# Kernel tuning notes

Measured on AMD Instinct MI355X. Metric: run time of the kernel, lower is better.

Reference implementation:

```python
import jax, jax.numpy as jnp
import numpy as np

B, D, L, R, O = 32768, 128, 3, 64, 64
EPS = 1e-5


def setup_inputs() -> dict:
    key = jax.random.key(0)
    ks = jax.random.split(key, 5)
    s_in = 1.0 / np.sqrt(D)
    s_r = 1.0 / np.sqrt(R)
    return {
        "x": jax.random.normal(ks[0], (B, D, L), dtype=jnp.float32),
        "layer0": jax.random.uniform(ks[1], (D, R), minval=-s_in, maxval=s_in, dtype=jnp.float32),
        "core1": jax.random.uniform(ks[2], (R, D, R), minval=-s_in, maxval=s_in, dtype=jnp.float32),
        "core2": jax.random.uniform(ks[3], (R, D, R), minval=-s_in, maxval=s_in, dtype=jnp.float32),
        "last": jax.random.uniform(ks[4], (R, O), minval=-s_r, maxval=s_r, dtype=jnp.float32),
        "ln_w": jnp.ones((D, L), dtype=jnp.float32),
        "ln_b": jnp.zeros((D, L), dtype=jnp.float32),
    }


def reference(x, layer0, core1, core2, last, ln_w, ln_b):
    # LayerNorm over the last two dims [D, L] with affine params
    mu = jnp.mean(x, axis=(1, 2), keepdims=True)
    var = jnp.var(x, axis=(1, 2), keepdims=True)
    xn = (x - mu) * jax.lax.rsqrt(var + EPS) * ln_w + ln_b  # [B, D, L]

    # Tensor-train contraction chain. The original builds a khatri-rao
    # [B, R*D] per step then matmuls with the reshaped [R*D, R] core;
    # einsum 'br,bd,rds->bs' computes the identical contraction fused.
    temp = xn[:, :, 0] @ layer0  # [B, R]
    temp = jnp.einsum("br,bd,rds->bs", temp, xn[:, :, 1], core1)
    temp = jnp.einsum("br,bd,rds->bs", temp, xn[:, :, 2], core2)
    return temp @ last  # [B, O]
```

## Files before the change

### kernel.cpp

```cpp
#include <hip/hip_runtime.h>
#include <hip/hip_fp16.h>

typedef _Float16 f16x8 __attribute__((ext_vector_type(8)));
typedef float f32x16 __attribute__((ext_vector_type(16)));

union H2x4 { f16x8 v; __half2 h2[4]; unsigned u[4]; };
union U1H2 { unsigned u; __half2 h; };

#define TB 128
#define XN0_OFF  0
#define RING_OFF 32768
#define T_OFF    65536
#define XN12_OFF 81920
#define SMEM_BYTES 148480
#define WS_CT1   0
#define WS_CT2   1048576
#define WS_L0T   2097152
#define WS_LASTT 2113536

#define WAITBAR0() asm volatile("s_waitcnt vmcnt(0)\n\ts_barrier" ::: "memory")

__device__ __forceinline__ void gload_lds16(const void* g, void* l) {
  __builtin_amdgcn_global_load_lds(
      (const __attribute__((address_space(1))) unsigned int*)g,
      (__attribute__((address_space(3))) unsigned int*)l, 16, 0, 0);
}

__device__ __forceinline__ void issue_chunk16(const unsigned char* g,
                                              unsigned char* l, int tid) {
  gload_lds16(g + tid * 16, l + tid * 16);
}

__device__ __forceinline__ unsigned pack_h2(float a, float b) {
  return (unsigned)__half_as_ushort(__float2half(a)) |
         ((unsigned)__half_as_ushort(__float2half(b)) << 16);
}

__device__ __forceinline__ void reduce_T(unsigned char* smem, f32x16 a0, f32x16 a1,
                                         int p, int kh, int mh, int h, int scol) {
  float* scr = (float*)(smem + (kh ? RING_OFF : XN0_OFF));
  __syncthreads();
  if (p == 0) {
#pragma unroll
    for (int j = 0; j < 16; ++j) {
      const int r0 = (j & 3) + 8 * (j >> 2) + 4 * h;
      const int row = mh * 64 + r0;
      scr[row * 64 + scol] = a0[j];
      scr[(row + 32) * 64 + scol] = a1[j];
    }
  }
  __syncthreads();
  if (p == 1) {
#pragma unroll
    for (int j = 0; j < 16; ++j) {
      const int r0 = (j & 3) + 8 * (j >> 2) + 4 * h;
      const int row = mh * 64 + r0;
      scr[row * 64 + scol] += a0[j];
      scr[(row + 32) * 64 + scol] += a1[j];
    }
  }
  __syncthreads();
  if (p == 0) {
    const float* s0 = (const float*)(smem + XN0_OFF);
    const float* s1 = (const float*)(smem + RING_OFF);
#pragma unroll
    for (int j = 0; j < 16; ++j) {
      const int r0 = (j & 3) + 8 * (j >> 2) + 4 * h;
      const int row = mh * 64 + kh * 32 + r0;
      const float vsum = s0[row * 64 + scol] + s1[row * 64 + scol];
      *(__half*)(smem + T_OFF + row * 128 + ((2 * scol) ^ ((row & 7) << 4))) =
          __float2half(vsum);
    }
  }
  __syncthreads();
}

__global__ void __launch_bounds__(512) tt_prep(
    const float* __restrict__ layer0, const float* __restrict__ core1,
    const float* __restrict__ core2, const float* __restrict__ last,
    unsigned char* __restrict__ ws) {
  const int tid = blockIdx.x * 512 + threadIdx.x;
  if (tid < 524288) {
    const int which = tid >> 18;
    const int w = tid & 262143;
    const float* core = which ? core2 : core1;
    unsigned char* ct = ws + (which ? WS_CT2 : WS_CT1);
    const int d = w >> 11, rem = w & 2047, s = rem >> 5, j = rem & 31, r = 2 * j;
    const unsigned val = pack_h2(core[r * 8192 + d * 64 + s],
                                 core[(r + 1) * 8192 + d * 64 + s]);
    *(unsigned*)(ct + d * 8192 + s * 128 + 4 * (j ^ ((s & 7) << 2))) = val;
  } else if (tid < 528384) {
    const int w = tid - 524288;
    const int r = w >> 6, j = w & 63, d = 2 * j;
    const unsigned val = pack_h2(layer0[d * 64 + r], layer0[(d + 1) * 64 + r]);
    *(unsigned*)(ws + WS_L0T + r * 256 + 4 * j) = val;
  } else if (tid < 530432) {
    const int w = tid - 528384;
    const int o = w >> 5, j = w & 31, r = 2 * j;
    const unsigned val = pack_h2(last[r * 64 + o], last[(r + 1) * 64 + o]);
    *(unsigned*)(ws + WS_LASTT + o * 128 + 4 * j) = val;
  }
}

__global__ void __launch_bounds__(1024, 4) tt_fused(
    const float* __restrict__ x, const float* __restrict__ lnw,
    const float* __restrict__ lnb, const unsigned char* __restrict__ ws,
    float* __restrict__ out) {
  __shared__ alignas(16) unsigned char smem[SMEM_BYTES];
  const int tid = threadIdx.x;
  const int wid = tid >> 6;
  const int lane = tid & 63;
  const int l31 = lane & 31;
  const int h = lane >> 5;
  const int p  = wid & 1;
  const int kh = (wid >> 1) & 1;
  const int sb = (wid >> 2) & 1;
  const int mh = (wid >> 3) & 1;
  const int bg0 = blockIdx.x * TB;
  const int scol = sb * 32 + l31;
  const int sOff = scol * 128;
  const int swzA = (l31 & 7) << 4;

  {
    float wv[6], bv[6];
#pragma unroll
    for (int k = 0; k < 6; ++k) { wv[k] = lnw[lane + 64 * k]; bv[k] = lnb[lane + 64 * k]; }
#pragma unroll
    for (int rr = 0; rr < 8; ++rr) {
      const int row = wid * 8 + rr;
      const float* xrow = x + (size_t)(bg0 + row) * 384;
      float v[6];
#pragma unroll
      for (int k = 0; k < 6; ++k) v[k] = xrow[lane + 64 * k];
      float s = 0.f, ss = 0.f;
#pragma unroll
      for (int k = 0; k < 6; ++k) { s += v[k]; ss += v[k] * v[k]; }
#pragma unroll
      for (int m = 1; m < 64; m <<= 1) { s += __shfl_xor(s, m); ss += __shfl_xor(ss, m); }
      const float mu = s * (1.f / 384.f);
      const float var = ss * (1.f / 384.f) - mu * mu;
      const float rstd = rsqrtf(var + 1e-5f);
#pragma unroll
      for (int k = 0; k < 6; ++k) {
        const int i = lane + 64 * k;
        const int d = i / 3;
        const int sl = i - 3 * d;
        const float xv = (v[k] - mu) * rstd * wv[k] + bv[k];
        if (sl == 0) {
          *(__half*)(smem + XN0_OFF + row * 256 + ((2 * d) ^ ((row & 7) << 4))) =
              __float2half(xv);
        } else {
          *(__half*)(smem + XN12_OFF + d * 520 + 4 * row + 2 * (sl - 1)) =
              __float2half(xv);
        }
      }
    }
  }
  __syncthreads();

  f32x16 acc0, acc1;

#pragma unroll
  for (int i = 0; i < 16; ++i) { acc0[i] = 0.f; acc1[i] = 0.f; }
  {
    const unsigned char* l0t = ws + WS_L0T;
#pragma unroll
    for (int kbL = 0; kbL < 2; ++kbL) {
      const int cb = (((p << 1) | kh) * 2 + kbL) * 32 + h * 16;
      f16x8 bf = *(const f16x8*)(l0t + scol * 256 + cb);
      f16x8 a0 = *(const f16x8*)(smem + XN0_OFF + (mh * 64 + l31) * 256 + (cb ^ swzA));
      f16x8 a1 = *(const f16x8*)(smem + XN0_OFF + (mh * 64 + 32 + l31) * 256 + (cb ^ swzA));
      acc0 = __builtin_amdgcn_mfma_f32_32x32x16_f16(a0, bf, acc0, 0, 0, 0);
      acc1 = __builtin_amdgcn_mfma_f32_32x32x16_f16(a1, bf, acc1, 0, 0, 0);
    }
  }
  reduce_T(smem, acc0, acc1, p, kh, mh, h, scol);

  for (int st = 0; st < 2; ++st) {
    const unsigned char* ctg = ws + (st ? WS_CT2 : WS_CT1);

    issue_chunk16(ctg, smem + RING_OFF, tid);

    H2x4 tp00, tp01, tp10, tp11;
    {
      const int rb0 = kh * 64 + h * 16;
      const int ra = (mh * 64 + l31) * 128;
      const int rb = (mh * 64 + 32 + l31) * 128;
      tp00.v = *(const f16x8*)(smem + T_OFF + ra + (rb0 ^ swzA));
      tp01.v = *(const f16x8*)(smem + T_OFF + ra + ((rb0 + 32) ^ swzA));
      tp10.v = *(const f16x8*)(smem + T_OFF + rb + (rb0 ^ swzA));
      tp11.v = *(const f16x8*)(smem + T_OFF + rb + ((rb0 + 32) ^ swzA));
    }

#pragma unroll
    for (int i = 0; i < 16; ++i) { acc0[i] = 0.f; acc1[i] = 0.f; }

#pragma unroll 1
    for (int cg = 0; cg < 64; ++cg) {
      WAITBAR0();
      if (cg < 63)
        issue_chunk16(ctg + (cg + 1) * 16384,
                      smem + RING_OFF + ((cg + 1) & 1) * 16384, tid);
      const unsigned char* bp =
          smem + RING_OFF + (cg & 1) * 16384 + p * 8192 + sOff;
      const unsigned char* xp = smem + XN12_OFF + (2 * cg + p) * 520 +
                                4 * (mh * 64 + l31) + 2 * st;
      const unsigned xv0 = *(const unsigned short*)xp;
      const unsigned xv1 = *(const unsigned short*)(xp + 128);
      U1H2 d0, d1;
      d0.u = xv0 | (xv0 << 16);
      d1.u = xv1 | (xv1 << 16);
      const int rb = kh * 64 + h * 16;
      {
        f16x8 bf = *(const f16x8*)(bp + (rb ^ swzA));
        H2x4 af0, af1;
#pragma unroll
        for (int i = 0; i < 4; ++i) {
          af0.h2[i] = __hmul2(tp00.h2[i], d0.h);
          af1.h2[i] = __hmul2(tp10.h2[i], d1.h);
        }
        acc0 = __builtin_amdgcn_mfma_f32_32x32x16_f16(af0.v, bf, acc0, 0, 0, 0);
        acc1 = __builtin_amdgcn_mfma_f32_32x32x16_f16(af1.v, bf, acc1, 0, 0, 0);
      }
      {
        f16x8 bf = *(const f16x8*)(bp + ((rb + 32) ^ swzA));
        H2x4 af0, af1;
#pragma unroll
        for (int i = 0; i < 4; ++i) {
          af0.h2[i] = __hmul2(tp01.h2[i], d0.h);
          af1.h2[i] = __hmul2(tp11.h2[i], d1.h);
        }
        acc0 = __builtin_amdgcn_mfma_f32_32x32x16_f16(af0.v, bf, acc0, 0, 0, 0);
        acc1 = __builtin_amdgcn_mfma_f32_32x32x16_f16(af1.v, bf, acc1, 0, 0, 0);
      }
    }
    reduce_T(smem, acc0, acc1, p, kh, mh, h, scol);
  }

  if (p == 0) {
    f32x16 accd;
#pragma unroll
    for (int i = 0; i < 16; ++i) accd[i] = 0.f;
    const unsigned char* lastT = ws + WS_LASTT;
    const int rbase = mh * 64 + kh * 32;
#pragma unroll
    for (int kb = 0; kb < 4; ++kb) {
      const int cb = kb * 32 + h * 16;
      f16x8 bf = *(const f16x8*)(lastT + scol * 128 + cb);
      f16x8 af = *(const f16x8*)(smem + T_OFF + (rbase + l31) * 128 + (cb ^ swzA));
      accd = __builtin_amdgcn_mfma_f32_32x32x16_f16(af, bf, accd, 0, 0, 0);
    }
#pragma unroll
    for (int j = 0; j < 16; ++j) {
      const int r0 = (j & 3) + 8 * (j >> 2) + 4 * h;
      out[(size_t)(bg0 + rbase + r0) * 64 + scol] = accd[j];
    }
  }
}

extern "C" void kernel_launch(void* const* d_in, const int* in_sizes, int n_in,
                              void* d_out, int out_size, void* d_ws, size_t ws_size,
                              hipStream_t stream) {
  const float* x      = (const float*)d_in[0];
  const float* layer0 = (const float*)d_in[1];
  const float* core1  = (const float*)d_in[2];
  const float* core2  = (const float*)d_in[3];
  const float* last   = (const float*)d_in[4];
  const float* lnw    = (const float*)d_in[5];
  const float* lnb    = (const float*)d_in[6];
  unsigned char* ws   = (unsigned char*)d_ws;
  float* outp         = (float*)d_out;

  tt_prep<<<1036, 512, 0, stream>>>(layer0, core1, core2, last, ws);
  tt_fused<<<256, 1024, 0, stream>>>(x, lnw, lnb, ws, outp);
}
```

Measured before the change: 101.5 us.

## Halve block to 512 threads with 4 M-tiles per wave and fragment-ordered core layout

```diff
diff --git a/kernel.cpp b/kernel.cpp
--- a/kernel.cpp
+++ b/kernel.cpp
@@ -29,6 +29,7 @@
 __device__ __forceinline__ void issue_chunk16(const unsigned char* g,
                                               unsigned char* l, int tid) {
   gload_lds16(g + tid * 16, l + tid * 16);
+  gload_lds16(g + tid * 16 + 8192, l + tid * 16 + 8192);
 }
 
 __device__ __forceinline__ unsigned pack_h2(float a, float b) {
@@ -36,17 +37,19 @@
          ((unsigned)__half_as_ushort(__float2half(b)) << 16);
 }
 
-__device__ __forceinline__ void reduce_T(unsigned char* smem, f32x16 a0, f32x16 a1,
-                                         int p, int kh, int mh, int h, int scol) {
+__device__ __forceinline__ void reduce_T(unsigned char* smem,
+                                         f32x16 a0, f32x16 a1, f32x16 a2, f32x16 a3,
+                                         int p, int kh, int h, int scol) {
   float* scr = (float*)(smem + (kh ? RING_OFF : XN0_OFF));
   __syncthreads();
   if (p == 0) {
 #pragma unroll
     for (int j = 0; j < 16; ++j) {
       const int r0 = (j & 3) + 8 * (j >> 2) + 4 * h;
-      const int row = mh * 64 + r0;
-      scr[row * 64 + scol] = a0[j];
-      scr[(row + 32) * 64 + scol] = a1[j];
+      scr[r0 * 64 + scol]        = a0[j];
+      scr[(32 + r0) * 64 + scol] = a1[j];
+      scr[(64 + r0) * 64 + scol] = a2[j];
+      scr[(96 + r0) * 64 + scol] = a3[j];
     }
   }
   __syncthreads();
@@ -54,9 +57,10 @@
 #pragma unroll
     for (int j = 0; j < 16; ++j) {
       const int r0 = (j & 3) + 8 * (j >> 2) + 4 * h;
-      const int row = mh * 64 + r0;
-      scr[row * 64 + scol] += a0[j];
-      scr[(row + 32) * 64 + scol] += a1[j];
+      scr[r0 * 64 + scol]        += a0[j];
+      scr[(32 + r0) * 64 + scol] += a1[j];
+      scr[(64 + r0) * 64 + scol] += a2[j];
+      scr[(96 + r0) * 64 + scol] += a3[j];
     }
   }
   __syncthreads();
@@ -66,8 +70,12 @@
 #pragma unroll
     for (int j = 0; j < 16; ++j) {
       const int r0 = (j & 3) + 8 * (j >> 2) + 4 * h;
-      const int row = mh * 64 + kh * 32 + r0;
-      const float vsum = s0[row * 64 + scol] + s1[row * 64 + scol];
+      int row = kh * 32 + r0;
+      float vsum = s0[row * 64 + scol] + s1[row * 64 + scol];
+      *(__half*)(smem + T_OFF + row * 128 + ((2 * scol) ^ ((row & 7) << 4))) =
+          __float2half(vsum);
+      row += 64;
+      vsum = s0[row * 64 + scol] + s1[row * 64 + scol];
       *(__half*)(smem + T_OFF + row * 128 + ((2 * scol) ^ ((row & 7) << 4))) =
           __float2half(vsum);
     }
@@ -85,10 +93,20 @@
     const int w = tid & 262143;
     const float* core = which ? core2 : core1;
     unsigned char* ct = ws + (which ? WS_CT2 : WS_CT1);
-    const int d = w >> 11, rem = w & 2047, s = rem >> 5, j = rem & 31, r = 2 * j;
-    const unsigned val = pack_h2(core[r * 8192 + d * 64 + s],
-                                 core[(r + 1) * 8192 + d * 64 + s]);
-    *(unsigned*)(ct + d * 8192 + s * 128 + 4 * (j ^ ((s & 7) << 2))) = val;
+    const int j   = w & 3;
+    const int lp  = (w >> 2) & 63;
+    const int blk = w >> 8;
+    const int kbL = blk & 1;
+    const int kh  = (blk >> 1) & 1;
+    const int sb  = (blk >> 2) & 1;
+    const int d   = blk >> 3;
+    const int hh  = lp & 1;
+    const int l31 = lp >> 1;
+    const int s   = sb * 32 + l31;
+    const int r0  = kh * 32 + kbL * 16 + hh * 8 + 2 * j;
+    const unsigned val = pack_h2(core[r0 * 8192 + d * 64 + s],
+                                 core[(r0 + 1) * 8192 + d * 64 + s]);
+    *(unsigned*)(ct + (size_t)w * 4) = val;
   } else if (tid < 528384) {
     const int w = tid - 524288;
     const int r = w >> 6, j = w & 63, d = 2 * j;
@@ -102,7 +120,18 @@
   }
 }
 
-__global__ void __launch_bounds__(1024, 4) tt_fused(
+#define KRSTEP(TPa, TPb, E, ACC)                                              \
+  do {                                                                        \
+    H2x4 af;                                                                  \
+    _Pragma("unroll") for (int q = 0; q < 4; ++q)                             \
+        af.h2[q] = __hmul2(TPa.h2[q], (E).h);                                 \
+    ACC = __builtin_amdgcn_mfma_f32_32x32x16_f16(af.v, bf0, ACC, 0, 0, 0);    \
+    _Pragma("unroll") for (int q = 0; q < 4; ++q)                             \
+        af.h2[q] = __hmul2(TPb.h2[q], (E).h);                                 \
+    ACC = __builtin_amdgcn_mfma_f32_32x32x16_f16(af.v, bf1, ACC, 0, 0, 0);    \
+  } while (0)
+
+__global__ void __launch_bounds__(512, 2) tt_fused(
     const float* __restrict__ x, const float* __restrict__ lnw,
     const float* __restrict__ lnb, const unsigned char* __restrict__ ws,
     float* __restrict__ out) {
@@ -115,10 +144,9 @@
   const int p  = wid & 1;
   const int kh = (wid >> 1) & 1;
   const int sb = (wid >> 2) & 1;
-  const int mh = (wid >> 3) & 1;
   const int bg0 = blockIdx.x * TB;
   const int scol = sb * 32 + l31;
-  const int sOff = scol * 128;
+  const int lp16 = (l31 * 2 + h) * 16;
   const int swzA = (l31 & 7) << 4;
 
   {
@@ -126,8 +154,8 @@
 #pragma unroll
     for (int k = 0; k < 6; ++k) { wv[k] = lnw[lane + 64 * k]; bv[k] = lnb[lane + 64 * k]; }
 #pragma unroll
-    for (int rr = 0; rr < 8; ++rr) {
-      const int row = wid * 8 + rr;
+    for (int rr = 0; rr < 16; ++rr) {
+      const int row = wid * 16 + rr;
       const float* xrow = x + (size_t)(bg0 + row) * 384;
       float v[6];
 #pragma unroll
@@ -158,42 +186,48 @@
   }
   __syncthreads();
 
-  f32x16 acc0, acc1;
-
-#pragma unroll
-  for (int i = 0; i < 16; ++i) { acc0[i] = 0.f; acc1[i] = 0.f; }
+  f32x16 acc0, acc1, acc2, acc3;
+
+#pragma unroll
+  for (int i = 0; i < 16; ++i) { acc0[i] = 0.f; acc1[i] = 0.f; acc2[i] = 0.f; acc3[i] = 0.f; }
   {
     const unsigned char* l0t = ws + WS_L0T;
 #pragma unroll
     for (int kbL = 0; kbL < 2; ++kbL) {
       const int cb = (((p << 1) | kh) * 2 + kbL) * 32 + h * 16;
       f16x8 bf = *(const f16x8*)(l0t + scol * 256 + cb);
-      f16x8 a0 = *(const f16x8*)(smem + XN0_OFF + (mh * 64 + l31) * 256 + (cb ^ swzA));
-      f16x8 a1 = *(const f16x8*)(smem + XN0_OFF + (mh * 64 + 32 + l31) * 256 + (cb ^ swzA));
-      acc0 = __builtin_amdgcn_mfma_f32_32x32x16_f16(a0, bf, acc0, 0, 0, 0);
-      acc1 = __builtin_amdgcn_mfma_f32_32x32x16_f16(a1, bf, acc1, 0, 0, 0);
-    }
-  }
-  reduce_T(smem, acc0, acc1, p, kh, mh, h, scol);
+      f16x8 aA = *(const f16x8*)(smem + XN0_OFF + l31 * 256 + (cb ^ swzA));
+      f16x8 aB = *(const f16x8*)(smem + XN0_OFF + (32 + l31) * 256 + (cb ^ swzA));
+      f16x8 aC = *(const f16x8*)(smem + XN0_OFF + (64 + l31) * 256 + (cb ^ swzA));
+      f16x8 aD = *(const f16x8*)(smem + XN0_OFF + (96 + l31) * 256 + (cb ^ swzA));
+      acc0 = __builtin_amdgcn_mfma_f32_32x32x16_f16(aA, bf, acc0, 0, 0, 0);
+      acc1 = __builtin_amdgcn_mfma_f32_32x32x16_f16(aB, bf, acc1, 0, 0, 0);
+      acc2 = __builtin_amdgcn_mfma_f32_32x32x16_f16(aC, bf, acc2, 0, 0, 0);
+      acc3 = __builtin_amdgcn_mfma_f32_32x32x16_f16(aD, bf, acc3, 0, 0, 0);
+    }
+  }
+  reduce_T(smem, acc0, acc1, acc2, acc3, p, kh, h, scol);
 
   for (int st = 0; st < 2; ++st) {
     const unsigned char* ctg = ws + (st ? WS_CT2 : WS_CT1);
 
     issue_chunk16(ctg, smem + RING_OFF, tid);
 
-    H2x4 tp00, tp01, tp10, tp11;
+    H2x4 tp00, tp01, tp10, tp11, tp20, tp21, tp30, tp31;
     {
       const int rb0 = kh * 64 + h * 16;
-      const int ra = (mh * 64 + l31) * 128;
-      const int rb = (mh * 64 + 32 + l31) * 128;
-      tp00.v = *(const f16x8*)(smem + T_OFF + ra + (rb0 ^ swzA));
-      tp01.v = *(const f16x8*)(smem + T_OFF + ra + ((rb0 + 32) ^ swzA));
-      tp10.v = *(const f16x8*)(smem + T_OFF + rb + (rb0 ^ swzA));
-      tp11.v = *(const f16x8*)(smem + T_OFF + rb + ((rb0 + 32) ^ swzA));
-    }
-
-#pragma unroll
-    for (int i = 0; i < 16; ++i) { acc0[i] = 0.f; acc1[i] = 0.f; }
+      tp00.v = *(const f16x8*)(smem + T_OFF + l31 * 128 + (rb0 ^ swzA));
+      tp01.v = *(const f16x8*)(smem + T_OFF + l31 * 128 + ((rb0 + 32) ^ swzA));
+      tp10.v = *(const f16x8*)(smem + T_OFF + (32 + l31) * 128 + (rb0 ^ swzA));
+      tp11.v = *(const f16x8*)(smem + T_OFF + (32 + l31) * 128 + ((rb0 + 32) ^ swzA));
+      tp20.v = *(const f16x8*)(smem + T_OFF + (64 + l31) * 128 + (rb0 ^ swzA));
+      tp21.v = *(const f16x8*)(smem + T_OFF + (64 + l31) * 128 + ((rb0 + 32) ^ swzA));
+      tp30.v = *(const f16x8*)(smem + T_OFF + (96 + l31) * 128 + (rb0 ^ swzA));
+      tp31.v = *(const f16x8*)(smem + T_OFF + (96 + l31) * 128 + ((rb0 + 32) ^ swzA));
+    }
+
+#pragma unroll
+    for (int i = 0; i < 16; ++i) { acc0[i] = 0.f; acc1[i] = 0.f; acc2[i] = 0.f; acc3[i] = 0.f; }
 
 #pragma unroll 1
     for (int cg = 0; cg < 64; ++cg) {
@@ -201,59 +235,48 @@
       if (cg < 63)
         issue_chunk16(ctg + (cg + 1) * 16384,
                       smem + RING_OFF + ((cg + 1) & 1) * 16384, tid);
-      const unsigned char* bp =
-          smem + RING_OFF + (cg & 1) * 16384 + p * 8192 + sOff;
+      const unsigned char* bp = smem + RING_OFF + (cg & 1) * 16384 +
+                                p * 8192 + sb * 4096 + kh * 2048 + lp16;
+      f16x8 bf0 = *(const f16x8*)(bp);
+      f16x8 bf1 = *(const f16x8*)(bp + 1024);
       const unsigned char* xp = smem + XN12_OFF + (2 * cg + p) * 520 +
-                                4 * (mh * 64 + l31) + 2 * st;
-      const unsigned xv0 = *(const unsigned short*)xp;
+                                4 * l31 + 2 * st;
+      const unsigned xv0 = *(const unsigned short*)(xp);
       const unsigned xv1 = *(const unsigned short*)(xp + 128);
-      U1H2 d0, d1;
-      d0.u = xv0 | (xv0 << 16);
-      d1.u = xv1 | (xv1 << 16);
-      const int rb = kh * 64 + h * 16;
-      {
-        f16x8 bf = *(const f16x8*)(bp + (rb ^ swzA));
-        H2x4 af0, af1;
-#pragma unroll
-        for (int i = 0; i < 4; ++i) {
-          af0.h2[i] = __hmul2(tp00.h2[i], d0.h);
-          af1.h2[i] = __hmul2(tp10.h2[i], d1.h);
-        }
-        acc0 = __builtin_amdgcn_mfma_f32_32x32x16_f16(af0.v, bf, acc0, 0, 0, 0);
-        acc1 = __builtin_amdgcn_mfma_f32_32x32x16_f16(af1.v, bf, acc1, 0, 0, 0);
-      }
-      {
-        f16x8 bf = *(const f16x8*)(bp + ((rb + 32) ^ swzA));
-        H2x4 af0, af1;
-#pragma unroll
-        for (int i = 0; i < 4; ++i) {
-          af0.h2[i] = __hmul2(tp01.h2[i], d0.h);
-          af1.h2[i] = __hmul2(tp11.h2[i], d1.h);
-        }
-        acc0 = __builtin_amdgcn_mfma_f32_32x32x16_f16(af0.v, bf, acc0, 0, 0, 0);
-        acc1 = __builtin_amdgcn_mfma_f32_32x32x16_f16(af1.v, bf, acc1, 0, 0, 0);
-      }
-    }
-    reduce_T(smem, acc0, acc1, p, kh, mh, h, scol);
+      const unsigned xv2 = *(const unsigned short*)(xp + 256);
+      const unsigned xv3 = *(const unsigned short*)(xp + 384);
+      U1H2 e0, e1, e2, e3;
+      e0.u = xv0 | (xv0 << 16);
+      e1.u = xv1 | (xv1 << 16);
+      e2.u = xv2 | (xv2 << 16);
+      e3.u = xv3 | (xv3 << 16);
+      KRSTEP(tp00, tp01, e0, acc0);
+      KRSTEP(tp10, tp11, e1, acc1);
+      KRSTEP(tp20, tp21, e2, acc2);
+      KRSTEP(tp30, tp31, e3, acc3);
+    }
+    reduce_T(smem, acc0, acc1, acc2, acc3, p, kh, h, scol);
   }
 
   if (p == 0) {
-    f32x16 accd;
-#pragma unroll
-    for (int i = 0; i < 16; ++i) accd[i] = 0.f;
+    f32x16 accd0, accd1;
+#pragma unroll
+    for (int i = 0; i < 16; ++i) { accd0[i] = 0.f; accd1[i] = 0.f; }
     const unsigned char* lastT = ws + WS_LASTT;
-    const int rbase = mh * 64 + kh * 32;
 #pragma unroll
     for (int kb = 0; kb < 4; ++kb) {
       const int cb = kb * 32 + h * 16;
       f16x8 bf = *(const f16x8*)(lastT + scol * 128 + cb);
-      f16x8 af = *(const f16x8*)(smem + T_OFF + (rbase + l31) * 128 + (cb ^ swzA));
-      accd = __builtin_amdgcn_mfma_f32_32x32x16_f16(af, bf, accd, 0, 0, 0);
-    }
-#pragma unroll
-    for (int j = 0; j < 16; ++j) {
-      const int r0 = (j & 3) + 8 * (j >> 2) + 4 * h;
-      out[(size_t)(bg0 + rbase + r0) * 64 + scol] = accd[j];
+      f16x8 af0 = *(const f16x8*)(smem + T_OFF + (kh * 32 + l31) * 128 + (cb ^ swzA));
+      f16x8 af1 = *(const f16x8*)(smem + T_OFF + (64 + kh * 32 + l31) * 128 + (cb ^ swzA));
+      accd0 = __builtin_amdgcn_mfma_f32_32x32x16_f16(af0, bf, accd0, 0, 0, 0);
+      accd1 = __builtin_amdgcn_mfma_f32_32x32x16_f16(af1, bf, accd1, 0, 0, 0);
+    }
+#pragma unroll
+    for (int j = 0; j < 16; ++j) {
+      const int r0 = (j & 3) + 8 * (j >> 2) + 4 * h;
+      out[(size_t)(bg0 + kh * 32 + r0) * 64 + scol] = accd0[j];
+      out[(size_t)(bg0 + 64 + kh * 32 + r0) * 64 + scol] = accd1[j];
     }
   }
 }
@@ -272,5 +295,5 @@
   float* outp         = (float*)d_out;
 
   tt_prep<<<1036, 512, 0, stream>>>(layer0, core1, core2, last, ws);
-  tt_fused<<<256, 1024, 0, stream>>>(x, lnw, lnb, ws, outp);
-}
+  tt_fused<<<256, 512, 0, stream>>>(x, lnw, lnb, ws, outp);
+}
```

Result: slower. 104.4 us (+2.9%).

## Pre-permute TT cores into MFMA fragment order and double chunk size

Applied to the files above, without the earlier changes.

```diff
diff --git a/kernel.cpp b/kernel.cpp
--- a/kernel.cpp
+++ b/kernel.cpp
@@ -8,10 +8,10 @@
 union U1H2 { unsigned u; __half2 h; };
 
 #define TB 128
-#define XN0_OFF  0
-#define RING_OFF 32768
-#define T_OFF    65536
-#define XN12_OFF 81920
+#define SLOT0_OFF 0
+#define SLOT1_OFF 32768
+#define T_OFF     65536
+#define XN12_OFF  81920
 #define SMEM_BYTES 148480
 #define WS_CT1   0
 #define WS_CT2   1048576
@@ -26,9 +26,10 @@
       (__attribute__((address_space(3))) unsigned int*)l, 16, 0, 0);
 }
 
-__device__ __forceinline__ void issue_chunk16(const unsigned char* g,
+__device__ __forceinline__ void issue_chunk32(const unsigned char* g,
                                               unsigned char* l, int tid) {
   gload_lds16(g + tid * 16, l + tid * 16);
+  gload_lds16(g + tid * 16 + 16384, l + tid * 16 + 16384);
 }
 
 __device__ __forceinline__ unsigned pack_h2(float a, float b) {
@@ -38,7 +39,7 @@
 
 __device__ __forceinline__ void reduce_T(unsigned char* smem, f32x16 a0, f32x16 a1,
                                          int p, int kh, int mh, int h, int scol) {
-  float* scr = (float*)(smem + (kh ? RING_OFF : XN0_OFF));
+  float* scr = (float*)(smem + (kh ? SLOT1_OFF : SLOT0_OFF));
   __syncthreads();
   if (p == 0) {
 #pragma unroll
@@ -61,8 +62,8 @@
   }
   __syncthreads();
   if (p == 0) {
-    const float* s0 = (const float*)(smem + XN0_OFF);
-    const float* s1 = (const float*)(smem + RING_OFF);
+    const float* s0 = (const float*)(smem + SLOT0_OFF);
+    const float* s1 = (const float*)(smem + SLOT1_OFF);
 #pragma unroll
     for (int j = 0; j < 16; ++j) {
       const int r0 = (j & 3) + 8 * (j >> 2) + 4 * h;
@@ -85,10 +86,20 @@
     const int w = tid & 262143;
     const float* core = which ? core2 : core1;
     unsigned char* ct = ws + (which ? WS_CT2 : WS_CT1);
-    const int d = w >> 11, rem = w & 2047, s = rem >> 5, j = rem & 31, r = 2 * j;
-    const unsigned val = pack_h2(core[r * 8192 + d * 64 + s],
-                                 core[(r + 1) * 8192 + d * 64 + s]);
-    *(unsigned*)(ct + d * 8192 + s * 128 + 4 * (j ^ ((s & 7) << 2))) = val;
+    const int j   = w & 3;
+    const int lp  = (w >> 2) & 63;
+    const int blk = w >> 8;
+    const int kbL = blk & 1;
+    const int kh  = (blk >> 1) & 1;
+    const int sb  = (blk >> 2) & 1;
+    const int d   = blk >> 3;
+    const int hh  = lp & 1;
+    const int l31 = lp >> 1;
+    const int s   = sb * 32 + l31;
+    const int r0  = kh * 32 + kbL * 16 + hh * 8 + 2 * j;
+    const unsigned val = pack_h2(core[r0 * 8192 + d * 64 + s],
+                                 core[(r0 + 1) * 8192 + d * 64 + s]);
+    *(unsigned*)(ct + (size_t)w * 4) = val;
   } else if (tid < 528384) {
     const int w = tid - 524288;
     const int r = w >> 6, j = w & 63, d = 2 * j;
@@ -118,7 +129,7 @@
   const int mh = (wid >> 3) & 1;
   const int bg0 = blockIdx.x * TB;
   const int scol = sb * 32 + l31;
-  const int sOff = scol * 128;
+  const int lp16 = (l31 * 2 + h) * 16;
   const int swzA = (l31 & 7) << 4;
 
   {
@@ -147,7 +158,7 @@
         const int sl = i - 3 * d;
         const float xv = (v[k] - mu) * rstd * wv[k] + bv[k];
         if (sl == 0) {
-          *(__half*)(smem + XN0_OFF + row * 256 + ((2 * d) ^ ((row & 7) << 4))) =
+          *(__half*)(smem + SLOT0_OFF + row * 256 + ((2 * d) ^ ((row & 7) << 4))) =
               __float2half(xv);
         } else {
           *(__half*)(smem + XN12_OFF + d * 520 + 4 * row + 2 * (sl - 1)) =
@@ -168,8 +179,8 @@
     for (int kbL = 0; kbL < 2; ++kbL) {
       const int cb = (((p << 1) | kh) * 2 + kbL) * 32 + h * 16;
       f16x8 bf = *(const f16x8*)(l0t + scol * 256 + cb);
-      f16x8 a0 = *(const f16x8*)(smem + XN0_OFF + (mh * 64 + l31) * 256 + (cb ^ swzA));
-      f16x8 a1 = *(const f16x8*)(smem + XN0_OFF + (mh * 64 + 32 + l31) * 256 + (cb ^ swzA));
+      f16x8 a0 = *(const f16x8*)(smem + SLOT0_OFF + (mh * 64 + l31) * 256 + (cb ^ swzA));
+      f16x8 a1 = *(const f16x8*)(smem + SLOT0_OFF + (mh * 64 + 32 + l31) * 256 + (cb ^ swzA));
       acc0 = __builtin_amdgcn_mfma_f32_32x32x16_f16(a0, bf, acc0, 0, 0, 0);
       acc1 = __builtin_amdgcn_mfma_f32_32x32x16_f16(a1, bf, acc1, 0, 0, 0);
     }
@@ -179,7 +190,7 @@
   for (int st = 0; st < 2; ++st) {
     const unsigned char* ctg = ws + (st ? WS_CT2 : WS_CT1);
 
-    issue_chunk16(ctg, smem + RING_OFF, tid);
+    issue_chunk32(ctg, smem + SLOT0_OFF, tid);
 
     H2x4 tp00, tp01, tp10, tp11;
     {
@@ -196,42 +207,45 @@
     for (int i = 0; i < 16; ++i) { acc0[i] = 0.f; acc1[i] = 0.f; }
 
 #pragma unroll 1
-    for (int cg = 0; cg < 64; ++cg) {
+    for (int cg = 0; cg < 32; ++cg) {
       WAITBAR0();
-      if (cg < 63)
-        issue_chunk16(ctg + (cg + 1) * 16384,
-                      smem + RING_OFF + ((cg + 1) & 1) * 16384, tid);
-      const unsigned char* bp =
-          smem + RING_OFF + (cg & 1) * 16384 + p * 8192 + sOff;
-      const unsigned char* xp = smem + XN12_OFF + (2 * cg + p) * 520 +
-                                4 * (mh * 64 + l31) + 2 * st;
-      const unsigned xv0 = *(const unsigned short*)xp;
-      const unsigned xv1 = *(const unsigned short*)(xp + 128);
-      U1H2 d0, d1;
-      d0.u = xv0 | (xv0 << 16);
-      d1.u = xv1 | (xv1 << 16);
-      const int rb = kh * 64 + h * 16;
-      {
-        f16x8 bf = *(const f16x8*)(bp + (rb ^ swzA));
-        H2x4 af0, af1;
-#pragma unroll
-        for (int i = 0; i < 4; ++i) {
-          af0.h2[i] = __hmul2(tp00.h2[i], d0.h);
-          af1.h2[i] = __hmul2(tp10.h2[i], d1.h);
+      if (cg < 31)
+        issue_chunk32(ctg + (cg + 1) * 32768,
+                      smem + ((cg + 1) & 1) * 32768, tid);
+      const unsigned char* chunk = smem + (cg & 1) * 32768;
+#pragma unroll
+      for (int dh = 0; dh < 2; ++dh) {
+        const int dloc = p + 2 * dh;
+        const unsigned char* bp = chunk + dloc * 8192 + sb * 4096 + kh * 2048 + lp16;
+        f16x8 bf0 = *(const f16x8*)(bp);
+        f16x8 bf1 = *(const f16x8*)(bp + 1024);
+        const unsigned char* xp = smem + XN12_OFF + (4 * cg + dloc) * 520 +
+                                  4 * (mh * 64 + l31) + 2 * st;
+        const unsigned xv0 = *(const unsigned short*)xp;
+        const unsigned xv1 = *(const unsigned short*)(xp + 128);
+        U1H2 e0, e1;
+        e0.u = xv0 | (xv0 << 16);
+        e1.u = xv1 | (xv1 << 16);
+        {
+          H2x4 af0, af1;
+#pragma unroll
+          for (int q = 0; q < 4; ++q) {
+            af0.h2[q] = __hmul2(tp00.h2[q], e0.h);
+            af1.h2[q] = __hmul2(tp10.h2[q], e1.h);
+          }
+          acc0 = __builtin_amdgcn_mfma_f32_32x32x16_f16(af0.v, bf0, acc0, 0, 0, 0);
+          acc1 = __builtin_amdgcn_mfma_f32_32x32x16_f16(af1.v, bf0, acc1, 0, 0, 0);
         }
-        acc0 = __builtin_amdgcn_mfma_f32_32x32x16_f16(af0.v, bf, acc0, 0, 0, 0);
-        acc1 = __builtin_amdgcn_mfma_f32_32x32x16_f16(af1.v, bf, acc1, 0, 0, 0);
-      }
-      {
-        f16x8 bf = *(const f16x8*)(bp + ((rb + 32) ^ swzA));
-        H2x4 af0, af1;
-#pragma unroll
-        for (int i = 0; i < 4; ++i) {
-          af0.h2[i] = __hmul2(tp01.h2[i], d0.h);
-          af1.h2[i] = __hmul2(tp11.h2[i], d1.h);
+        {
+          H2x4 af0, af1;
+#pragma unroll
+          for (int q = 0; q < 4; ++q) {
+            af0.h2[q] = __hmul2(tp01.h2[q], e0.h);
+            af1.h2[q] = __hmul2(tp11.h2[q], e1.h);
+          }
+          acc0 = __builtin_amdgcn_mfma_f32_32x32x16_f16(af0.v, bf1, acc0, 0, 0, 0);
+          acc1 = __builtin_amdgcn_mfma_f32_32x32x16_f16(af1.v, bf1, acc1, 0, 0, 0);
         }
-        acc0 = __builtin_amdgcn_mfma_f32_32x32x16_f16(af0.v, bf, acc0, 0, 0, 0);
-        acc1 = __builtin_amdgcn_mfma_f32_32x32x16_f16(af1.v, bf, acc1, 0, 0, 0);
       }
     }
     reduce_T(smem, acc0, acc1, p, kh, mh, h, scol);
```

Measured after the change: 98.58 us. 2.9% less time.
